# Kernel tuning notes

Measured on AMD Instinct MI355X. Metric: run time of the kernel, lower is better.

Reference implementation:

```python
import jax, jax.numpy as jnp
import numpy as np

N, IN_DIM, D, H, E_DIM, G, NPG = 512, 16, 256, 8, 6, 32, 16
C = D           # per-head channels in GATv2Conv/TransformerConv (out_channels=d_model)
HD = D // H     # MultiheadAttention head dim


def _ln(x, g, b, eps=1e-5):
    m = jnp.mean(x, -1, keepdims=True)
    v = jnp.mean((x - m) ** 2, -1, keepdims=True)
    return (x - m) * jax.lax.rsqrt(v + eps) * g + b


def _seg_softmax(logits, seg, n):
    # numerically stable softmax over edges grouped by destination node
    m = jax.ops.segment_max(logits, seg, num_segments=n)
    m = jnp.where(jnp.isfinite(m), m, 0.0)
    e = jnp.exp(logits - m[seg])
    s = jax.ops.segment_sum(e, seg, num_segments=n)
    return e / jnp.maximum(s[seg], 1e-16)


def _forward(x, edge_attr, emb_w, emb_b, emb_g, emb_bb, pe, gat_lw, gat_lb, gat_rw, gat_rb, gat_ew, gat_att, gat_bias, tq_w, tq_b, tk_w, tk_b, tv_w, tv_b, te_w, tskip_w, tskip_b, tbeta_w, ln_g, ln_b, mha_in_w, mha_in_b, mha_out_w, mha_out_b, pool_w, pool_b, c1_w, c1_b, c1_g, c1_bb, rb_w, rb_b, rb_g, rb_bb, c2_w, c2_b, edge_index, batch):
    src, dst = edge_index[0], edge_index[1]
    E = edge_attr.shape[0]
    # input embedding (Linear + LayerNorm) + learned positional encoding (eval: no dropout)
    h = _ln(x @ emb_w.T + emb_b, emb_g, emb_bb) + pe[:N]
    residual = h
    # --- GATv2Conv(d_model, d_model, heads=H, edge_dim=6, concat=False, add_self_loops=False) ---
    xl = (h @ gat_lw.T + gat_lb).reshape(N, H, C)          # source transform
    xr = (h @ gat_rw.T + gat_rb).reshape(N, H, C)          # target transform
    ee = (edge_attr @ gat_ew.T).reshape(E, H, C)
    z = jax.nn.leaky_relu(xl[src] + xr[dst] + ee, 0.2)
    a = _seg_softmax(jnp.einsum('ehc,hc->eh', z, gat_att), dst, N)
    x_gat = jax.ops.segment_sum(xl[src] * a[..., None], dst, num_segments=N).mean(1) + gat_bias
    x_gat = _ln(x_gat, ln_g, ln_b)
    # --- TransformerConv(d_model, d_model, heads=H, edge_dim=6, concat=False, beta=True) ---
    te = (edge_attr @ te_w.T).reshape(E, H, C)
    q = (x_gat @ tq_w.T + tq_b).reshape(N, H, C)[dst]
    k = (x_gat @ tk_w.T + tk_b).reshape(N, H, C)[src] + te
    v = (x_gat @ tv_w.T + tv_b).reshape(N, H, C)[src] + te
    a2 = _seg_softmax((q * k).sum(-1) / np.sqrt(C).astype(np.float32), dst, N)
    out = jax.ops.segment_sum(v * a2[..., None], dst, num_segments=N).mean(1)
    r = x_gat @ tskip_w.T + tskip_b
    beta = jax.nn.sigmoid(jnp.concatenate([out, r, out - r], -1) @ tbeta_w.T)
    x_tr = _ln(beta * r + (1.0 - beta) * out, ln_g, ln_b)
    # --- dynamic attention mask: after the repeat/permute/reshape gymnastics this equals
    #     ds[:N] repeated H*N times, reshaped to [H, N, N] ---
    im = edge_attr[:, 5]
    ds = jnp.exp(-0.5 * ((im - 125.09) / 15.0) ** 2)
    ds = 1.0 - (ds - ds.min()) / (ds.max() - ds.min())
    mask = jnp.repeat(ds[:N], H * N).reshape(H, N, N)
    # --- cross MultiheadAttention (query=x_tr, key=x_gat, value=h, attn_mask added) ---
    wq, wk, wv = jnp.split(mha_in_w, 3, axis=0)
    bq, bk, bv = jnp.split(mha_in_b, 3, axis=0)
    qh = ((x_tr @ wq.T + bq) / np.sqrt(HD).astype(np.float32)).reshape(N, H, HD).transpose(1, 0, 2)
    kh = (x_gat @ wk.T + bk).reshape(N, H, HD).transpose(1, 0, 2)
    vh = (h @ wv.T + bv).reshape(N, H, HD).transpose(1, 0, 2)
    attn = jax.nn.softmax(qh @ kh.transpose(0, 2, 1) + mask, axis=-1)   # [H,N,N]
    o = (attn @ vh).transpose(1, 0, 2).reshape(N, D) @ mha_out_w.T + mha_out_b
    # torch broadcast of [N,1,D] attn output + [N,D] residual -> [N,N,D]
    x3 = o[:, None, :] + residual[None, :, :]
    # attention pooling: softmax over a size-1 dim yields all-ones scores (kept faithfully)
    x2 = x3.reshape(N * N, D)
    brep = jnp.tile(batch, N)
    score = jax.nn.softmax(x2 @ pool_w.T + pool_b, axis=1)
    pooled = jax.ops.segment_sum(score * x2, brep, num_segments=G)
    # classifier: Linear->LN->GELU->ResidualBlockv2->Linear (dropout off in eval)
    c = jax.nn.gelu(_ln(pooled @ c1_w.T + c1_b, c1_g, c1_bb), approximate=False)
    c = c + jax.nn.gelu(_ln(c @ rb_w.T + rb_b, rb_g, rb_bb), approximate=False)
    return c @ c2_w.T + c2_b   # [G, 1]


def setup_inputs():
    key = jax.random.key(0)
    ks = iter(jax.random.split(key, 64))
    f = lambda *sh: 0.02 * jax.random.normal(next(ks), sh, jnp.float32)
    # G fully-connected directed cliques of NPG nodes (no self loops) -> every node has in-edges
    i = np.arange(NPG)
    s, t = np.meshgrid(i, i, indexing='ij')
    msk = s != t
    s, t = s[msk], t[msk]
    off = (np.arange(G) * NPG)[:, None]
    edge_index = jnp.asarray(np.stack([(s[None] + off).reshape(-1), (t[None] + off).reshape(-1)]), jnp.int32)
    E = edge_index.shape[1]
    batch = jnp.asarray(np.repeat(np.arange(G), NPG), jnp.int32)
    x = jax.random.normal(next(ks), (N, IN_DIM), jnp.float32)
    edge_attr = jax.random.normal(next(ks), (E, E_DIM), jnp.float32)
    edge_attr = edge_attr.at[:, 5].set(edge_attr[:, 5] * 30.0 + 125.0)  # invariant-mass-like column
    HC = H * C
    return dict(
        x=x, edge_attr=edge_attr,
        emb_w=f(D, IN_DIM), emb_b=f(D), emb_g=jnp.ones(D), emb_bb=jnp.zeros(D),
        pe=f(1000, D),
        gat_lw=f(HC, D), gat_lb=f(HC), gat_rw=f(HC, D), gat_rb=f(HC),
        gat_ew=f(HC, E_DIM), gat_att=f(H, C), gat_bias=f(C),
        tq_w=f(HC, D), tq_b=f(HC), tk_w=f(HC, D), tk_b=f(HC),
        tv_w=f(HC, D), tv_b=f(HC), te_w=f(HC, E_DIM),
        tskip_w=f(D, D), tskip_b=f(D), tbeta_w=f(1, 3 * D),
        ln_g=jnp.ones(D), ln_b=jnp.zeros(D),
        mha_in_w=f(3 * D, D), mha_in_b=f(3 * D), mha_out_w=f(D, D), mha_out_b=f(D),
        pool_w=f(1, D), pool_b=f(1),
        c1_w=f(128, D), c1_b=f(128), c1_g=jnp.ones(128), c1_bb=jnp.zeros(128),
        rb_w=f(128, 128), rb_b=f(128), rb_g=jnp.ones(128), rb_bb=jnp.zeros(128),
        c2_w=f(1, 128), c2_b=f(1),
        edge_index=edge_index, batch=batch)


def reference(x, edge_attr, emb_w, emb_b, emb_g, emb_bb, pe, gat_lw, gat_lb, gat_rw, gat_rb, gat_ew, gat_att, gat_bias, tq_w, tq_b, tk_w, tk_b, tv_w, tv_b, te_w, tskip_w, tskip_b, tbeta_w, ln_g, ln_b, mha_in_w, mha_in_b, mha_out_w, mha_out_b, pool_w, pool_b, c1_w, c1_b, c1_g, c1_bb, rb_w, rb_b, rb_g, rb_bb, c2_w, c2_b, edge_index, batch):
    return _forward(x, edge_attr, emb_w, emb_b, emb_g, emb_bb, pe, gat_lw, gat_lb, gat_rw, gat_rb, gat_ew, gat_att, gat_bias, tq_w, tq_b, tk_w, tk_b, tv_w, tv_b, te_w, tskip_w, tskip_b, tbeta_w, ln_g, ln_b, mha_in_w, mha_in_b, mha_out_w, mha_out_b, pool_w, pool_b, c1_w, c1_b, c1_g, c1_bb, rb_w, rb_b, rb_g, rb_bb, c2_w, c2_b, edge_index, batch)
```

## Files before the change

### kernel.cpp

```cpp
#include <hip/hip_runtime.h>
#include <hip/hip_bf16.h>
#include <math.h>

#define NN 512
#define DM 256
#define NH 8
#define NG 32
#define NPG 16
#define INDIM 16
#define BIGW (2048 * 256)

typedef __hip_bfloat16 bf16;
typedef __attribute__((ext_vector_type(8))) short short8;
typedef __attribute__((ext_vector_type(4))) float f32x4;

__device__ __forceinline__ float b2f(bf16 v) { return __bfloat162float(v); }
__device__ __forceinline__ bf16 f2b(float v) { return __float2bfloat16(v); }
__device__ __forceinline__ short f2bs(float v) { bf16 t = __float2bfloat16(v); return *(short*)&t; }
__device__ __forceinline__ float fin(float v) {
    return (v == v && v > -1e30f && v < 1e30f) ? v : 0.f;
}
__device__ __forceinline__ int is_bf16(const void* ones_arr) {
    return ((const unsigned short*)ones_arr)[0] == 0x3F80u;
}

__device__ __forceinline__ void unpack8(uint4 u, float* w) {
    unsigned uu[4] = {u.x, u.y, u.z, u.w};
    #pragma unroll
    for (int j = 0; j < 4; j++) {
        __hip_bfloat162 b2 = *reinterpret_cast<const __hip_bfloat162*>(&uu[j]);
        float2 f = __bfloat1622float2(b2);
        w[2 * j] = f.x; w[2 * j + 1] = f.y;
    }
}
__device__ __forceinline__ float4 bload4(const bf16* p) {
    uint2 u = *(const uint2*)p;
    __hip_bfloat162 a = *reinterpret_cast<const __hip_bfloat162*>(&u.x);
    __hip_bfloat162 b = *reinterpret_cast<const __hip_bfloat162*>(&u.y);
    float2 f0 = __bfloat1622float2(a), f1 = __bfloat1622float2(b);
    return make_float4(f0.x, f0.y, f1.x, f1.y);
}

__device__ __forceinline__ float dot256(const float* xrow, const bf16* wrow) {
    const uint4* w4 = (const uint4*)wrow;
    uint4 q = w4[0];
    float acc = 0.f;
    for (int k8 = 0; k8 < 32; k8++) {
        uint4 qn = w4[(k8 + 1) & 31];
        float w[8]; unpack8(q, w);
        const float4* sp = (const float4*)&xrow[k8 * 8];
        float4 a0 = sp[0], a1 = sp[1];
        acc += a0.x*w[0] + a0.y*w[1] + a0.z*w[2] + a0.w*w[3]
             + a1.x*w[4] + a1.y*w[5] + a1.z*w[6] + a1.w*w[7];
        q = qn;
    }
    return acc;
}

template<int BS>
__device__ __forceinline__ float ln_norm(float v, float g, float b, float* red) {
    int t = threadIdx.x;
    red[t] = v; __syncthreads();
    for (int s = BS / 2; s > 0; s >>= 1) { if (t < s) red[t] += red[t + s]; __syncthreads(); }
    float mean = red[0] * (1.0f / (float)BS); __syncthreads();
    float d = v - mean;
    red[t] = d * d; __syncthreads();
    for (int s = BS / 2; s > 0; s >>= 1) { if (t < s) red[t] += red[t + s]; __syncthreads(); }
    float var = red[0] * (1.0f / (float)BS); __syncthreads();
    return d * rsqrtf(var + 1e-5f) * g + b;
}

struct CvtTab { const void* p[35]; int cum[36]; };
__global__ void k_convert(CvtTab tab, const void* ones, bf16* wbuf) {
    int i = blockIdx.x * 256 + threadIdx.x;
    if (i >= tab.cum[35]) return;
    int bf = is_bf16(ones);
    int a = 0;
    while (i >= tab.cum[a + 1]) a++;
    int off = i - tab.cum[a];
    float v = bf ? b2f(((const bf16*)tab.p[a])[off]) : ((const float*)tab.p[a])[off];
    wbuf[i] = f2b(v);
}

struct Cvt5 { const void* p[5]; };
__global__ void k_convert_big(Cvt5 tab, const void* ones, bf16* wbig) {
    int i = blockIdx.x * 256 + threadIdx.x;
    int a = blockIdx.y;
    int bf = is_bf16(ones);
    float v = bf ? b2f(((const bf16*)tab.p[a])[i]) : ((const float*)tab.p[a])[i];
    wbig[(size_t)a * BIGW + i] = f2b(v);
}

__global__ void k_embed(const bf16* xw, const bf16* emw, const bf16* emb, const bf16* emg,
                        const bf16* embb, const bf16* pe, float* h,
                        float* pre1, float* pre2) {
    int n = blockIdx.x, t = threadIdx.x;
    size_t gi = (size_t)n * DM + t;
    pre1[gi] = 0.f;
    pre2[gi] = 0.f;
    __shared__ float xin[INDIM];
    __shared__ float red[DM];
    if (t < INDIM) xin[t] = b2f(xw[n * INDIM + t]);
    __syncthreads();
    float acc = b2f(emb[t]);
    #pragma unroll
    for (int k = 0; k < INDIM; k++) acc += xin[k] * b2f(emw[t * INDIM + k]);
    float y = ln_norm<DM>(acc, b2f(emg[t]), b2f(embb[t]), red);
    h[gi] = fin(y + b2f(pe[gi]));
}

__device__ __forceinline__ void row_softmax16(float* M, int tid) {
    if (tid < NPG) {
        float* row = M + tid * NPG;
        float m = -1e30f;
        #pragma unroll
        for (int s = 0; s < NPG; s++) m = fmaxf(m, row[s]);
        if (m < -1e29f) {
            #pragma unroll
            for (int s = 0; s < NPG; s++) row[s] = 0.f;
        } else {
            float sum = 0.f;
            #pragma unroll
            for (int s = 0; s < NPG; s++) sum += expf(row[s] - m);
            float inv = 1.f / fmaxf(sum, 1e-16f);
            #pragma unroll
            for (int s = 0; s < NPG; s++) row[s] = expf(row[s] - m) * inv;
        }
    }
}

__global__ __launch_bounds__(256, 1)
void k_gat_fused(const float* h, const bf16* lw, const bf16* rw,
                 const bf16* lb, const bf16* rbv, const bf16* eww, const bf16* attw,
                 const bf16* ea, const int* src, const int* dst, int epg, float* pre) {
    extern __shared__ char smraw[];
    int g = blockIdx.x, hh = blockIdx.y, tid = threadIdx.x;
    bf16* hb     = (bf16*)smraw;
    float* ew_s  = (float*)(hb + NPG * DM);
    float* att_s = ew_s + 6 * DM;
    float* ea_s  = att_s + DM;
    float* Mx    = ea_s + 6 * epg;
    int* sl_s    = (int*)(Mx + NPG * NPG);
    int* dl_s    = sl_s + epg;
    bf16* xl_s   = (bf16*)(dl_s + epg);
    bf16* xr_s   = xl_s + NPG * DM;

    int ebase = g * epg;
    for (int i = tid; i < NPG * DM; i += 256) hb[i] = f2b(h[(size_t)g * NPG * DM + i]);
    for (int i = tid; i < 6 * DM; i += 256) {
        int f = i >> 8, cc = i & 255;
        ew_s[f * DM + cc] = b2f(eww[(size_t)(hh * DM + cc) * 6 + f]);
    }
    att_s[tid] = b2f(attw[hh * DM + tid]);
    for (int i = tid; i < 6 * epg; i += 256) {
        int f = i / epg, e = i - f * epg;
        ea_s[f * epg + e] = b2f(ea[(size_t)(ebase + e) * 6 + f]);
    }
    if (tid < NPG * NPG) Mx[tid] = -1e30f;
    if (tid < epg) {
        int e = ebase + tid;
        sl_s[tid] = (src[e] - g * NPG) & (NPG - 1);
        dl_s[tid] = (dst[e] - g * NPG) & (NPG - 1);
    }
    __syncthreads();

    int lane = tid & 63, wave = tid >> 6;
    int n16 = lane & 15, quad = lane >> 4;
    f32x4 accA[4], accB[4];
    #pragma unroll
    for (int ct = 0; ct < 4; ct++) { accA[ct] = (f32x4)0.f; accB[ct] = (f32x4)0.f; }
    for (int ks = 0; ks < 8; ks++) {
        short8 a8 = *(const short8*)&hb[n16 * DM + ks * 32 + quad * 8];
        #pragma unroll
        for (int ct = 0; ct < 4; ct++) {
            int col = (ct * 4 + wave) * 16 + n16;
            size_t wo = (size_t)(hh * DM + col) * DM + ks * 32 + quad * 8;
            short8 bL = *(const short8*)(lw + wo);
            short8 bR = *(const short8*)(rw + wo);
            accA[ct] = __builtin_amdgcn_mfma_f32_16x16x32_bf16(a8, bL, accA[ct], 0, 0, 0);
            accB[ct] = __builtin_amdgcn_mfma_f32_16x16x32_bf16(a8, bR, accB[ct], 0, 0, 0);
        }
    }
    #pragma unroll
    for (int ct = 0; ct < 4; ct++) {
        int col = (ct * 4 + wave) * 16 + n16;
        float blv = b2f(lb[hh * DM + col]), brv = b2f(rbv[hh * DM + col]);
        #pragma unroll
        for (int reg = 0; reg < 4; reg++) {
            int row = quad * 4 + reg;
            xl_s[row * DM + col] = f2b(accA[ct][reg] + blv);
            xr_s[row * DM + col] = f2b(accB[ct][reg] + brv);
        }
    }
    __syncthreads();

    int c4 = lane * 4;
    for (int ei = wave; ei < epg; ei += 4) {
        int sl = sl_s[ei], dl = dl_s[ei];
        float ee0 = 0.f, ee1 = 0.f, ee2 = 0.f, ee3 = 0.f;
        #pragma unroll
        for (int f = 0; f < 6; f++) {
            float eb = ea_s[f * epg + ei];
            float4 wf = *(const float4*)&ew_s[f * DM + c4];
            ee0 += eb * wf.x; ee1 += eb * wf.y; ee2 += eb * wf.z; ee3 += eb * wf.w;
        }
        float4 av = *(const float4*)&att_s[c4];
        float4 xlv = bload4(&xl_s[sl * DM + c4]);
        float4 xrv = bload4(&xr_s[dl * DM + c4]);
        float z0 = xlv.x + xrv.x + ee0;
        float z1 = xlv.y + xrv.y + ee1;
        float z2 = xlv.z + xrv.z + ee2;
        float z3 = xlv.w + xrv.w + ee3;
        z0 = (z0 >= 0.f) ? z0 : 0.2f * z0;
        z1 = (z1 >= 0.f) ? z1 : 0.2f * z1;
        z2 = (z2 >= 0.f) ? z2 : 0.2f * z2;
        z3 = (z3 >= 0.f) ? z3 : 0.2f * z3;
        float acc = z0 * av.x + z1 * av.y + z2 * av.z + z3 * av.w;
        #pragma unroll
        for (int off = 32; off > 0; off >>= 1) acc += __shfl_down(acc, off);
        if (lane == 0) Mx[dl * NPG + sl] = fin(acc);
    }
    __syncthreads();
    row_softmax16(Mx, tid);
    __syncthreads();

    int c = tid;
    float xlv[NPG];
    #pragma unroll
    for (int s = 0; s < NPG; s++) xlv[s] = b2f(xl_s[s * DM + c]);
    #pragma unroll
    for (int d = 0; d < NPG; d++) {
        const float* Ar = Mx + d * NPG;
        float acc = 0.f;
        #pragma unroll
        for (int s = 0; s < NPG; s++) acc += Ar[s] * xlv[s];
        atomicAdd(&pre[(size_t)(g * NPG + d) * DM + c], fin(acc));
    }
}

__global__ void k_gat_post_skip(const float* pre, const bf16* gat_bias, const bf16* lng,
                                const bf16* lnb, const bf16* skw, const bf16* skb,
                                float* x_gat, float* rbuf) {
    int n = blockIdx.x, t = threadIdx.x;
    __shared__ float red[DM];
    __shared__ float xrow[DM];
    float v = pre[(size_t)n * DM + t] * 0.125f + b2f(gat_bias[t]);
    float y = fin(ln_norm<DM>(v, b2f(lng[t]), b2f(lnb[t]), red));
    x_gat[(size_t)n * DM + t] = y;
    xrow[t] = y;
    __syncthreads();
    rbuf[(size_t)n * DM + t] = fin(dot256(xrow, skw + (size_t)t * DM) + b2f(skb[t]));
}

__global__ __launch_bounds__(256, 1)
void k_tr_fused(const float* xg, const bf16* qw, const bf16* kw, const bf16* vw,
                const bf16* qb, const bf16* kb, const bf16* vb, const bf16* tew,
                const bf16* ea, const int* src, const int* dst, int epg, float* pre) {
    extern __shared__ char smraw[];
    int g = blockIdx.x, hh = blockIdx.y, tid = threadIdx.x;
    bf16* hb    = (bf16*)smraw;
    float* tw_s = (float*)(hb + NPG * DM);
    float* ea_s = tw_s + 6 * DM;
    float* Lqk  = ea_s + 6 * epg;
    float* Mx   = Lqk + NPG * NPG;
    float* P    = Mx + NPG * NPG;
    float* W6   = P + NPG * 6;
    int* emap   = (int*)(W6 + NPG * 6);
    int* sl_s   = emap + NPG * NPG;
    int* dl_s   = sl_s + epg;
    bf16* q_s   = (bf16*)(dl_s + epg);
    bf16* k_s   = q_s + NPG * DM;
    bf16* v_s   = k_s + NPG * DM;

    int ebase = g * epg;
    for (int i = tid; i < NPG * DM; i += 256) hb[i] = f2b(xg[(size_t)g * NPG * DM + i]);
    for (int i = tid; i < 6 * DM; i += 256) {
        int f = i >> 8, cc = i & 255;
        tw_s[f * DM + cc] = b2f(tew[(size_t)(hh * DM + cc) * 6 + f]);
    }
    for (int i = tid; i < 6 * epg; i += 256) {
        int f = i / epg, e = i - f * epg;
        ea_s[f * epg + e] = b2f(ea[(size_t)(ebase + e) * 6 + f]);
    }
    if (tid < NPG * NPG) { Mx[tid] = -1e30f; emap[tid] = -1; }
    if (tid < epg) {
        int e = ebase + tid;
        sl_s[tid] = (src[e] - g * NPG) & (NPG - 1);
        dl_s[tid] = (dst[e] - g * NPG) & (NPG - 1);
    }
    __syncthreads();

    int lane = tid & 63, wave = tid >> 6;
    int n16 = lane & 15, quad = lane >> 4;
    f32x4 aQ[4], aK[4], aV[4];
    #pragma unroll
    for (int ct = 0; ct < 4; ct++) { aQ[ct] = (f32x4)0.f; aK[ct] = (f32x4)0.f; aV[ct] = (f32x4)0.f; }
    for (int ks = 0; ks < 8; ks++) {
        short8 a8 = *(const short8*)&hb[n16 * DM + ks * 32 + quad * 8];
        #pragma unroll
        for (int ct = 0; ct < 4; ct++) {
            int col = (ct * 4 + wave) * 16 + n16;
            size_t wo = (size_t)(hh * DM + col) * DM + ks * 32 + quad * 8;
            short8 bQ = *(const short8*)(qw + wo);
            short8 bK = *(const short8*)(kw + wo);
            short8 bV = *(const short8*)(vw + wo);
            aQ[ct] = __builtin_amdgcn_mfma_f32_16x16x32_bf16(a8, bQ, aQ[ct], 0, 0, 0);
            aK[ct] = __builtin_amdgcn_mfma_f32_16x16x32_bf16(a8, bK, aK[ct], 0, 0, 0);
            aV[ct] = __builtin_amdgcn_mfma_f32_16x16x32_bf16(a8, bV, aV[ct], 0, 0, 0);
        }
    }
    #pragma unroll
    for (int ct = 0; ct < 4; ct++) {
        int col = (ct * 4 + wave) * 16 + n16;
        float bq = b2f(qb[hh * DM + col]), bk = b2f(kb[hh * DM + col]), bv = b2f(vb[hh * DM + col]);
        #pragma unroll
        for (int reg = 0; reg < 4; reg++) {
            int row = quad * 4 + reg;
            q_s[row * DM + col] = f2b(aQ[ct][reg] + bq);
            k_s[row * DM + col] = f2b(aK[ct][reg] + bk);
            v_s[row * DM + col] = f2b(aV[ct][reg] + bv);
        }
    }
    __syncthreads();

    if (wave == 0) {
        f32x4 acc = (f32x4)0.f;
        for (int ks = 0; ks < 8; ks++) {
            short8 a8 = *(const short8*)&q_s[n16 * DM + ks * 32 + quad * 8];
            short8 b8 = *(const short8*)&k_s[n16 * DM + ks * 32 + quad * 8];
            acc = __builtin_amdgcn_mfma_f32_16x16x32_bf16(a8, b8, acc, 0, 0, 0);
        }
        #pragma unroll
        for (int reg = 0; reg < 4; reg++)
            Lqk[(quad * 4 + reg) * NPG + n16] = acc[reg];
    } else if (wave <= 2) {
        int idx = tid - 64;
        if (idx < NPG * 6) {
            int d = idx / 6, f = idx - d * 6;
            const bf16* qr = q_s + d * DM;
            const float* twr = tw_s + f * DM;
            float acc = 0.f;
            for (int cc = 0; cc < DM; cc += 4) {
                float4 qv = bload4(qr + cc);
                float4 t4 = *(const float4*)(twr + cc);
                acc += qv.x * t4.x + qv.y * t4.y + qv.z * t4.z + qv.w * t4.w;
            }
            P[idx] = acc;
        }
    }
    __syncthreads();

    if (tid < epg) {
        int sl = sl_s[tid], dl = dl_s[tid];
        float acc = Lqk[dl * NPG + sl];
        #pragma unroll
        for (int f = 0; f < 6; f++) acc += ea_s[f * epg + tid] * P[dl * 6 + f];
        Mx[dl * NPG + sl] = fin(acc * 0.0625f);
        emap[dl * NPG + sl] = tid;
    }
    __syncthreads();
    row_softmax16(Mx, tid);
    __syncthreads();
    if (tid < NPG * 6) {
        int d = tid / 6, f = tid - d * 6;
        float acc = 0.f;
        #pragma unroll
        for (int s = 0; s < NPG; s++) {
            int e = emap[d * NPG + s];
            if (e >= 0) acc += Mx[d * NPG + s] * ea_s[f * epg + e];
        }
        W6[tid] = acc;
    }
    __syncthreads();

    int c = tid;
    float vv[NPG];
    #pragma unroll
    for (int s = 0; s < NPG; s++) vv[s] = b2f(v_s[s * DM + c]);
    float twc[6];
    #pragma unroll
    for (int f = 0; f < 6; f++) twc[f] = tw_s[f * DM + c];
    #pragma unroll
    for (int d = 0; d < NPG; d++) {
        const float* Ar = Mx + d * NPG;
        const float* Wr = W6 + d * 6;
        float acc = 0.f;
        #pragma unroll
        for (int s = 0; s < NPG; s++) acc += Ar[s] * vv[s];
        #pragma unroll
        for (int f = 0; f < 6; f++) acc += Wr[f] * twc[f];
        atomicAdd(&pre[(size_t)(g * NPG + d) * DM + c], fin(acc));
    }
}

__global__ void k_tr_post_qkv(const float* pre, const float* rbuf, const float* x_gat,
                              const float* h, const bf16* tbeta, const bf16* lng,
                              const bf16* lnb, const bf16* mw, const bf16* mb, float* qkv) {
    int n = blockIdx.x, t = threadIdx.x;
    __shared__ float red[DM];
    __shared__ float xtr_s[DM];
    __shared__ float xg_s[DM];
    __shared__ float h_s[DM];
    __shared__ float beta_sh;
    float outc = pre[(size_t)n * DM + t] * 0.125f;
    float rc = rbuf[(size_t)n * DM + t];
    xg_s[t] = x_gat[(size_t)n * DM + t];
    h_s[t] = h[(size_t)n * DM + t];
    float w1 = b2f(tbeta[t]), w2 = b2f(tbeta[DM + t]), w3 = b2f(tbeta[2 * DM + t]);
    red[t] = outc * (w1 + w3) + rc * (w2 - w3);
    __syncthreads();
    for (int s2 = 128; s2 > 0; s2 >>= 1) { if (t < s2) red[t] += red[t + s2]; __syncthreads(); }
    if (t == 0) beta_sh = 1.0f / (1.0f + expf(-red[0]));
    __syncthreads();
    float beta = beta_sh;
    float mix = beta * rc + (1.0f - beta) * outc;
    float y = fin(ln_norm<DM>(mix, b2f(lng[t]), b2f(lnb[t]), red));
    xtr_s[t] = y;
    __syncthreads();
    float q = (dot256(xtr_s, mw + (size_t)t * DM) + b2f(mb[t])) * 0.17677669529663689f;
    float k = dot256(xg_s, mw + (size_t)(DM + t) * DM) + b2f(mb[DM + t]);
    float v = dot256(h_s, mw + (size_t)(2 * DM + t) * DM) + b2f(mb[2 * DM + t]);
    qkv[(size_t)n * DM + t] = fin(q);
    qkv[((size_t)NN + n) * DM + t] = fin(k);
    qkv[((size_t)2 * NN + n) * DM + t] = fin(v);
}

#define KPAD 40
#define SPAD 516
__global__ __launch_bounds__(256, 1)
void k_attn(const float* qh, const float* kh, const float* vh, float* ao) {
    extern __shared__ char sm[];
    bf16* qb   = (bf16*)sm;
    bf16* KV   = qb + 16 * 32;
    float* Sc  = (float*)(KV + 256 * KPAD);
    float* Op  = Sc + 16 * SPAD;
    float* red = Op + 4 * 16 * 32;
    int qt = blockIdx.x, hd = blockIdx.y, tid = threadIdx.x;
    int lane = tid & 63, wave = tid >> 6, n16 = lane & 15, quad = lane >> 4;

    for (int i = tid; i < 16 * 32; i += 256)
        qb[i] = f2b(qh[(size_t)(qt * 16 + (i >> 5)) * DM + hd * 32 + (i & 31)]);

    for (int half = 0; half < 2; half++) {
        __syncthreads();
        for (int i = tid; i < 256 * 32; i += 256) {
            int j = i >> 5, d = i & 31;
            KV[j * KPAD + d] = f2b(kh[(size_t)(half * 256 + j) * DM + hd * 32 + d]);
        }
        __syncthreads();
        short8 a8 = *(const short8*)&qb[n16 * 32 + quad * 8];
        #pragma unroll
        for (int it = 0; it < 4; it++) {
            int ktl = wave * 4 + it;
            short8 b8 = *(const short8*)&KV[(ktl * 16 + n16) * KPAD + quad * 8];
            f32x4 acc = (f32x4)0.f;
            acc = __builtin_amdgcn_mfma_f32_16x16x32_bf16(a8, b8, acc, 0, 0, 0);
            #pragma unroll
            for (int reg = 0; reg < 4; reg++)
                Sc[(quad * 4 + reg) * SPAD + half * 256 + ktl * 16 + n16] = acc[reg];
        }
    }
    __syncthreads();

    int r = tid >> 4, li = tid & 15;
    float m = -1e30f;
    for (int s = 0; s < 32; s++) m = fmaxf(m, Sc[r * SPAD + li + 16 * s]);
    red[r * 16 + li] = m; __syncthreads();
    for (int st = 8; st > 0; st >>= 1) {
        if (li < st) red[r * 16 + li] = fmaxf(red[r * 16 + li], red[r * 16 + li + st]);
        __syncthreads();
    }
    m = red[r * 16];
    __syncthreads();
    float sum = 0.f;
    for (int s = 0; s < 32; s++) sum += expf(Sc[r * SPAD + li + 16 * s] - m);
    red[r * 16 + li] = sum; __syncthreads();
    for (int st = 8; st > 0; st >>= 1) {
        if (li < st) red[r * 16 + li] += red[r * 16 + li + st];
        __syncthreads();
    }
    float inv = 1.0f / fmaxf(red[r * 16], 1e-16f);
    for (int s = 0; s < 32; s++) {
        int idx = r * SPAD + li + 16 * s;
        Sc[idx] = expf(Sc[idx] - m) * inv;
    }

    f32x4 o0 = (f32x4)0.f, o1 = (f32x4)0.f;
    for (int half = 0; half < 2; half++) {
        __syncthreads();
        for (int i = tid; i < 256 * 32; i += 256) {
            int j = i >> 5, d = i & 31;
            KV[j * KPAD + d] = f2b(vh[(size_t)(half * 256 + j) * DM + hd * 32 + d]);
        }
        __syncthreads();
        #pragma unroll
        for (int it = 0; it < 2; it++) {
            int ksl = wave * 2 + it;
            int ks = half * 8 + ksl;
            const float* sp = &Sc[n16 * SPAD + ks * 32 + quad * 8];
            float4 s0 = *(const float4*)sp, s1 = *((const float4*)sp + 1);
            short8 a8;
            a8[0] = f2bs(s0.x); a8[1] = f2bs(s0.y); a8[2] = f2bs(s0.z); a8[3] = f2bs(s0.w);
            a8[4] = f2bs(s1.x); a8[5] = f2bs(s1.y); a8[6] = f2bs(s1.z); a8[7] = f2bs(s1.w);
            short8 bv0, bv1;
            #pragma unroll
            for (int j = 0; j < 8; j++) {
                bf16 t0 = KV[(ksl * 32 + quad * 8 + j) * KPAD + n16];
                bf16 t1 = KV[(ksl * 32 + quad * 8 + j) * KPAD + 16 + n16];
                bv0[j] = *(short*)&t0;
                bv1[j] = *(short*)&t1;
            }
            o0 = __builtin_amdgcn_mfma_f32_16x16x32_bf16(a8, bv0, o0, 0, 0, 0);
            o1 = __builtin_amdgcn_mfma_f32_16x16x32_bf16(a8, bv1, o1, 0, 0, 0);
        }
    }
    #pragma unroll
    for (int reg = 0; reg < 4; reg++) {
        Op[wave * 512 + (quad * 4 + reg) * 32 + n16] = o0[reg];
        Op[wave * 512 + (quad * 4 + reg) * 32 + 16 + n16] = o1[reg];
    }
    __syncthreads();
    for (int e = tid; e < 512; e += 256) {
        float v = Op[e] + Op[512 + e] + Op[1024 + e] + Op[1536 + e];
        ao[(size_t)(qt * 16 + (e >> 5)) * DM + hd * 32 + (e & 31)] = fin(v);
    }
}

__global__ void k_outproj(const float* ao, const bf16* W, const bf16* B, float* obuf) {
    int n = blockIdx.x, t = threadIdx.x;
    __shared__ float xrow[DM];
    xrow[t] = ao[(size_t)n * DM + t];
    __syncthreads();
    obuf[(size_t)n * DM + t] = fin(dot256(xrow, W + (size_t)t * DM) + b2f(B[t]));
}

__global__ void k_pool_sums(const float* o, const float* h, float* gsum_o, float* gsum_h) {
    int g = blockIdx.x, which = blockIdx.y, t = threadIdx.x;
    const float* src = which ? h : o;
    float acc = 0.f;
    #pragma unroll
    for (int j = 0; j < NPG; j++) acc += src[(size_t)(g * NPG + j) * DM + t];
    (which ? gsum_h : gsum_o)[g * DM + t] = fin(acc);
}

__global__ void k_mlp(const float* gsum_o, const float* gsum_h,
                      const bf16* c1_w, const bf16* c1_b, const bf16* c1_g,
                      const bf16* c1_bb, const bf16* rb_w, const bf16* rb_b,
                      const bf16* rb_g, const bf16* rb_bb, const bf16* c2_w,
                      const bf16* c2_b, const void* ones, void* out) {
    int g = blockIdx.x, t = threadIdx.x;
    __shared__ float pl[DM];
    __shared__ float u[128];
    __shared__ float red[128];
    float os0 = 0.f, os1 = 0.f;
    #pragma unroll
    for (int b = 0; b < NG; b++) {
        os0 += gsum_o[b * DM + t];
        os1 += gsum_o[b * DM + t + 128];
    }
    pl[t]       = fin((float)NPG * os0 + (float)NN * gsum_h[g * DM + t]);
    pl[t + 128] = fin((float)NPG * os1 + (float)NN * gsum_h[g * DM + t + 128]);
    __syncthreads();
    float acc = dot256(pl, c1_w + (size_t)t * DM) + b2f(c1_b[t]);
    float y = ln_norm<128>(acc, b2f(c1_g[t]), b2f(c1_bb[t]), red);
    float gl = 0.5f * y * (1.0f + erff(y * 0.70710678118654752f));
    u[t] = gl; __syncthreads();
    float acc2 = b2f(rb_b[t]);
    for (int k = 0; k < 128; k++) acc2 += u[k] * b2f(rb_w[(size_t)t * 128 + k]);
    float y2 = ln_norm<128>(acc2, b2f(rb_g[t]), b2f(rb_bb[t]), red);
    float cfin = gl + 0.5f * y2 * (1.0f + erff(y2 * 0.70710678118654752f));
    red[t] = cfin * b2f(c2_w[t]);
    __syncthreads();
    for (int s2 = 64; s2 > 0; s2 >>= 1) { if (t < s2) red[t] += red[t + s2]; __syncthreads(); }
    if (t == 0) {
        float res = fin(red[0] + b2f(c2_b[0]));
        if (is_bf16(ones)) ((bf16*)out)[g] = f2b(res);
        else               ((float*)out)[g] = res;
    }
}

extern "C" void kernel_launch(void* const* d_in, const int* in_sizes, int n_in,
                              void* d_out, int out_size, void* d_ws, size_t ws_size,
                              hipStream_t stream) {
    const int E = in_sizes[1] / 6;
    const int epg = E / NG;
    const int* eidx = (const int*)d_in[42];
    const int* srcp = eidx;
    const int* dstp = eidx + E;
    const void* ones = d_in[4];

    static const int idxs[35] = {0,1,2,3,4,5,6,8,10,11,12,13,15,17,19,20,21,22,23,24,
                                 25,26,27,28,29,32,33,34,35,36,37,38,39,40,41};
    CvtTab tab;
    int wOff[44];
    int cum = 0;
    for (int a = 0; a < 35; a++) {
        tab.p[a] = d_in[idxs[a]];
        tab.cum[a] = cum;
        wOff[idxs[a]] = cum;
        cum += in_sizes[idxs[a]];
    }
    tab.cum[35] = cum;
    const int totalW = cum;
    Cvt5 tab5;
    tab5.p[0] = d_in[7];  tab5.p[1] = d_in[9];
    tab5.p[2] = d_in[14]; tab5.p[3] = d_in[16]; tab5.p[4] = d_in[18];

    bf16* wbuf = (bf16*)d_ws;
    size_t wbytes = ((size_t)totalW * 2 + 255) & ~(size_t)255;
    float* fb = (float*)((char*)d_ws + wbytes);
    const size_t SL = (size_t)NN * DM;
    float* h      = fb;
    float* x_gat  = fb + SL;
    float* rbuf   = fb + 2 * SL;
    float* pre1   = fb + 3 * SL;
    float* pre2   = fb + 4 * SL;
    float* qkv    = fb + 5 * SL;
    float* gsum_o = fb + 8 * SL;
    float* gsum_h = gsum_o + NG * DM;
    bf16* wbig = (bf16*)qkv;
    float* ao = pre1;
    float* obuf = pre2;

    #define WB(i) (wbuf + wOff[i])

    k_convert<<<(totalW + 255) / 256, 256, 0, stream>>>(tab, ones, wbuf);
    k_convert_big<<<dim3(BIGW / 256, 5), 256, 0, stream>>>(tab5, ones, wbig);

    k_embed<<<NN, DM, 0, stream>>>(WB(0), WB(2), WB(3), WB(4), WB(5), WB(6), h, pre1, pre2);

    int gat_lds = NPG*DM*2 + (6*DM + DM + 6*epg + NPG*NPG) * 4 + (2*epg) * 4
                + 2*NPG*DM*2 + 16;
    k_gat_fused<<<dim3(NG, NH), 256, gat_lds, stream>>>(
        h, wbig, wbig + BIGW, WB(8), WB(10), WB(11), WB(12), WB(1), srcp, dstp, epg, pre1);
    k_gat_post_skip<<<NN, DM, 0, stream>>>(pre1, WB(13), WB(24), WB(25), WB(21), WB(22),
                                           x_gat, rbuf);

    int tr_lds = NPG*DM*2 + (6*DM + 6*epg + 2*NPG*NPG + 2*NPG*6) * 4
               + (NPG*NPG + 2*epg) * 4 + 3*NPG*DM*2 + 16;
    k_tr_fused<<<dim3(NG, NH), 256, tr_lds, stream>>>(
        x_gat, wbig + 2 * (size_t)BIGW, wbig + 3 * (size_t)BIGW, wbig + 4 * (size_t)BIGW,
        WB(15), WB(17), WB(19), WB(20), WB(1), srcp, dstp, epg, pre2);
    k_tr_post_qkv<<<NN, DM, 0, stream>>>(pre2, rbuf, x_gat, h, WB(23), WB(24), WB(25),
                                         WB(26), WB(27), qkv);

    int attn_lds = 16*32*2 + 256*KPAD*2 + 16*SPAD*4 + 4*16*32*4 + 16*16*4;
    k_attn<<<dim3(NN / 16, NH), 256, attn_lds, stream>>>(qkv, qkv + SL, qkv + 2 * SL, ao);
    k_outproj<<<NN, DM, 0, stream>>>(ao, WB(28), WB(29), obuf);

    k_pool_sums<<<dim3(NG, 2), DM, 0, stream>>>(obuf, h, gsum_o, gsum_h);
    k_mlp<<<NG, 128, 0, stream>>>(gsum_o, gsum_h, WB(32), WB(33), WB(34), WB(35),
                                  WB(36), WB(37), WB(38), WB(39), WB(40), WB(41),
                                  ones, d_out);
    #undef WB
}
```

Baseline: 321.7 us.

## Double GAT/Transformer conv block threads and fold pooling sums into producers

The fused GAT and TransformerConv kernels now launch 512 threads per block instead of 256. The MFMA column tiles, edge loop and aggregation loop are split across 8 waves, and the edge and attention weights are kept in LDS as bf16 to shrink shared memory. The separate pooling-sum kernel is removed: per-graph sums of h and of the output projection are accumulated with atomicAdd in the embed and outproj kernels, and the accumulators are zeroed inside the convert kernel. This cuts one launch and raises per-block parallelism, at the cost of atomic contention and non-deterministic summation order.

```diff
diff --git a/kernel.cpp b/kernel.cpp
--- a/kernel.cpp
+++ b/kernel.cpp
@@ -71,15 +71,18 @@
 }
 
 struct CvtTab { const void* p[35]; int cum[36]; };
-__global__ void k_convert(CvtTab tab, const void* ones, bf16* wbuf) {
+__global__ void k_convert(CvtTab tab, const void* ones, bf16* wbuf, float* gz, int nz) {
     int i = blockIdx.x * 256 + threadIdx.x;
-    if (i >= tab.cum[35]) return;
-    int bf = is_bf16(ones);
-    int a = 0;
-    while (i >= tab.cum[a + 1]) a++;
-    int off = i - tab.cum[a];
-    float v = bf ? b2f(((const bf16*)tab.p[a])[off]) : ((const float*)tab.p[a])[off];
-    wbuf[i] = f2b(v);
+    if (i < tab.cum[35]) {
+        int bf = is_bf16(ones);
+        int a = 0;
+        while (i >= tab.cum[a + 1]) a++;
+        int off = i - tab.cum[a];
+        float v = bf ? b2f(((const bf16*)tab.p[a])[off]) : ((const float*)tab.p[a])[off];
+        wbuf[i] = f2b(v);
+    } else if (i < tab.cum[35] + nz) {
+        gz[i - tab.cum[35]] = 0.f;
+    }
 }
 
 struct Cvt5 { const void* p[5]; };
@@ -93,7 +96,7 @@
 
 __global__ void k_embed(const bf16* xw, const bf16* emw, const bf16* emb, const bf16* emg,
                         const bf16* embb, const bf16* pe, float* h,
-                        float* pre1, float* pre2) {
+                        float* pre1, float* pre2, float* gsum_h) {
     int n = blockIdx.x, t = threadIdx.x;
     size_t gi = (size_t)n * DM + t;
     pre1[gi] = 0.f;
@@ -106,7 +109,9 @@
     #pragma unroll
     for (int k = 0; k < INDIM; k++) acc += xin[k] * b2f(emw[t * INDIM + k]);
     float y = ln_norm<DM>(acc, b2f(emg[t]), b2f(embb[t]), red);
-    h[gi] = fin(y + b2f(pe[gi]));
+    float hv = fin(y + b2f(pe[gi]));
+    h[gi] = hv;
+    atomicAdd(&gsum_h[(n >> 4) * DM + t], hv);
 }
 
 __device__ __forceinline__ void row_softmax16(float* M, int tid) {
@@ -129,16 +134,16 @@
     }
 }
 
-__global__ __launch_bounds__(256, 1)
+__global__ __launch_bounds__(512, 1)
 void k_gat_fused(const float* h, const bf16* lw, const bf16* rw,
                  const bf16* lb, const bf16* rbv, const bf16* eww, const bf16* attw,
                  const bf16* ea, const int* src, const int* dst, int epg, float* pre) {
     extern __shared__ char smraw[];
     int g = blockIdx.x, hh = blockIdx.y, tid = threadIdx.x;
     bf16* hb     = (bf16*)smraw;
-    float* ew_s  = (float*)(hb + NPG * DM);
-    float* att_s = ew_s + 6 * DM;
-    float* ea_s  = att_s + DM;
+    bf16* ew_s   = hb + NPG * DM;
+    bf16* att_s  = ew_s + 6 * DM;
+    float* ea_s  = (float*)(att_s + DM);
     float* Mx    = ea_s + 6 * epg;
     int* sl_s    = (int*)(Mx + NPG * NPG);
     int* dl_s    = sl_s + epg;
@@ -146,13 +151,13 @@
     bf16* xr_s   = xl_s + NPG * DM;
 
     int ebase = g * epg;
-    for (int i = tid; i < NPG * DM; i += 256) hb[i] = f2b(h[(size_t)g * NPG * DM + i]);
-    for (int i = tid; i < 6 * DM; i += 256) {
+    for (int i = tid; i < NPG * DM; i += 512) hb[i] = f2b(h[(size_t)g * NPG * DM + i]);
+    for (int i = tid; i < 6 * DM; i += 512) {
         int f = i >> 8, cc = i & 255;
-        ew_s[f * DM + cc] = b2f(eww[(size_t)(hh * DM + cc) * 6 + f]);
-    }
-    att_s[tid] = b2f(attw[hh * DM + tid]);
-    for (int i = tid; i < 6 * epg; i += 256) {
+        ew_s[f * DM + cc] = eww[(size_t)(hh * DM + cc) * 6 + f];
+    }
+    if (tid < DM) att_s[tid] = attw[hh * DM + tid];
+    for (int i = tid; i < 6 * epg; i += 512) {
         int f = i / epg, e = i - f * epg;
         ea_s[f * epg + e] = b2f(ea[(size_t)(ebase + e) * 6 + f]);
     }
@@ -166,14 +171,14 @@
 
     int lane = tid & 63, wave = tid >> 6;
     int n16 = lane & 15, quad = lane >> 4;
-    f32x4 accA[4], accB[4];
-    #pragma unroll
-    for (int ct = 0; ct < 4; ct++) { accA[ct] = (f32x4)0.f; accB[ct] = (f32x4)0.f; }
+    f32x4 accA[2], accB[2];
+    #pragma unroll
+    for (int ct = 0; ct < 2; ct++) { accA[ct] = (f32x4)0.f; accB[ct] = (f32x4)0.f; }
     for (int ks = 0; ks < 8; ks++) {
         short8 a8 = *(const short8*)&hb[n16 * DM + ks * 32 + quad * 8];
         #pragma unroll
-        for (int ct = 0; ct < 4; ct++) {
-            int col = (ct * 4 + wave) * 16 + n16;
+        for (int ct = 0; ct < 2; ct++) {
+            int col = (ct * 8 + wave) * 16 + n16;
             size_t wo = (size_t)(hh * DM + col) * DM + ks * 32 + quad * 8;
             short8 bL = *(const short8*)(lw + wo);
             short8 bR = *(const short8*)(rw + wo);
@@ -182,8 +187,8 @@
         }
     }
     #pragma unroll
-    for (int ct = 0; ct < 4; ct++) {
-        int col = (ct * 4 + wave) * 16 + n16;
+    for (int ct = 0; ct < 2; ct++) {
+        int col = (ct * 8 + wave) * 16 + n16;
         float blv = b2f(lb[hh * DM + col]), brv = b2f(rbv[hh * DM + col]);
         #pragma unroll
         for (int reg = 0; reg < 4; reg++) {
@@ -195,16 +200,16 @@
     __syncthreads();
 
     int c4 = lane * 4;
-    for (int ei = wave; ei < epg; ei += 4) {
+    for (int ei = wave; ei < epg; ei += 8) {
         int sl = sl_s[ei], dl = dl_s[ei];
         float ee0 = 0.f, ee1 = 0.f, ee2 = 0.f, ee3 = 0.f;
         #pragma unroll
         for (int f = 0; f < 6; f++) {
             float eb = ea_s[f * epg + ei];
-            float4 wf = *(const float4*)&ew_s[f * DM + c4];
+            float4 wf = bload4(&ew_s[f * DM + c4]);
             ee0 += eb * wf.x; ee1 += eb * wf.y; ee2 += eb * wf.z; ee3 += eb * wf.w;
         }
-        float4 av = *(const float4*)&att_s[c4];
+        float4 av = bload4(&att_s[c4]);
         float4 xlv = bload4(&xl_s[sl * DM + c4]);
         float4 xrv = bload4(&xr_s[dl * DM + c4]);
         float z0 = xlv.x + xrv.x + ee0;
@@ -224,12 +229,13 @@
     row_softmax16(Mx, tid);
     __syncthreads();
 
-    int c = tid;
+    int c = tid & 255, halfd = tid >> 8;
     float xlv[NPG];
     #pragma unroll
     for (int s = 0; s < NPG; s++) xlv[s] = b2f(xl_s[s * DM + c]);
     #pragma unroll
-    for (int d = 0; d < NPG; d++) {
+    for (int dd = 0; dd < 8; dd++) {
+        int d = halfd * 8 + dd;
         const float* Ar = Mx + d * NPG;
         float acc = 0.f;
         #pragma unroll
@@ -252,15 +258,15 @@
     rbuf[(size_t)n * DM + t] = fin(dot256(xrow, skw + (size_t)t * DM) + b2f(skb[t]));
 }
 
-__global__ __launch_bounds__(256, 1)
+__global__ __launch_bounds__(512, 1)
 void k_tr_fused(const float* xg, const bf16* qw, const bf16* kw, const bf16* vw,
                 const bf16* qb, const bf16* kb, const bf16* vb, const bf16* tew,
                 const bf16* ea, const int* src, const int* dst, int epg, float* pre) {
     extern __shared__ char smraw[];
     int g = blockIdx.x, hh = blockIdx.y, tid = threadIdx.x;
     bf16* hb    = (bf16*)smraw;
-    float* tw_s = (float*)(hb + NPG * DM);
-    float* ea_s = tw_s + 6 * DM;
+    bf16* tw_s  = hb + NPG * DM;
+    float* ea_s = (float*)(tw_s + 6 * DM);
     float* Lqk  = ea_s + 6 * epg;
     float* Mx   = Lqk + NPG * NPG;
     float* P    = Mx + NPG * NPG;
@@ -273,12 +279,12 @@
     bf16* v_s   = k_s + NPG * DM;
 
     int ebase = g * epg;
-    for (int i = tid; i < NPG * DM; i += 256) hb[i] = f2b(xg[(size_t)g * NPG * DM + i]);
-    for (int i = tid; i < 6 * DM; i += 256) {
+    for (int i = tid; i < NPG * DM; i += 512) hb[i] = f2b(xg[(size_t)g * NPG * DM + i]);
+    for (int i = tid; i < 6 * DM; i += 512) {
         int f = i >> 8, cc = i & 255;
-        tw_s[f * DM + cc] = b2f(tew[(size_t)(hh * DM + cc) * 6 + f]);
-    }
-    for (int i = tid; i < 6 * epg; i += 256) {
+        tw_s[f * DM + cc] = tew[(size_t)(hh * DM + cc) * 6 + f];
+    }
+    for (int i = tid; i < 6 * epg; i += 512) {
         int f = i / epg, e = i - f * epg;
         ea_s[f * epg + e] = b2f(ea[(size_t)(ebase + e) * 6 + f]);
     }
@@ -292,14 +298,14 @@
 
     int lane = tid & 63, wave = tid >> 6;
     int n16 = lane & 15, quad = lane >> 4;
-    f32x4 aQ[4], aK[4], aV[4];
-    #pragma unroll
-    for (int ct = 0; ct < 4; ct++) { aQ[ct] = (f32x4)0.f; aK[ct] = (f32x4)0.f; aV[ct] = (f32x4)0.f; }
+    f32x4 aQ[2], aK[2], aV[2];
+    #pragma unroll
+    for (int ct = 0; ct < 2; ct++) { aQ[ct] = (f32x4)0.f; aK[ct] = (f32x4)0.f; aV[ct] = (f32x4)0.f; }
     for (int ks = 0; ks < 8; ks++) {
         short8 a8 = *(const short8*)&hb[n16 * DM + ks * 32 + quad * 8];
         #pragma unroll
-        for (int ct = 0; ct < 4; ct++) {
-            int col = (ct * 4 + wave) * 16 + n16;
+        for (int ct = 0; ct < 2; ct++) {
+            int col = (ct * 8 + wave) * 16 + n16;
             size_t wo = (size_t)(hh * DM + col) * DM + ks * 32 + quad * 8;
             short8 bQ = *(const short8*)(qw + wo);
             short8 bK = *(const short8*)(kw + wo);
@@ -310,8 +316,8 @@
         }
     }
     #pragma unroll
-    for (int ct = 0; ct < 4; ct++) {
-        int col = (ct * 4 + wave) * 16 + n16;
+    for (int ct = 0; ct < 2; ct++) {
+        int col = (ct * 8 + wave) * 16 + n16;
         float bq = b2f(qb[hh * DM + col]), bk = b2f(kb[hh * DM + col]), bv = b2f(vb[hh * DM + col]);
         #pragma unroll
         for (int reg = 0; reg < 4; reg++) {
@@ -338,11 +344,11 @@
         if (idx < NPG * 6) {
             int d = idx / 6, f = idx - d * 6;
             const bf16* qr = q_s + d * DM;
-            const float* twr = tw_s + f * DM;
+            const bf16* twr = tw_s + f * DM;
             float acc = 0.f;
             for (int cc = 0; cc < DM; cc += 4) {
                 float4 qv = bload4(qr + cc);
-                float4 t4 = *(const float4*)(twr + cc);
+                float4 t4 = bload4(twr + cc);
                 acc += qv.x * t4.x + qv.y * t4.y + qv.z * t4.z + qv.w * t4.w;
             }
             P[idx] = acc;
@@ -373,15 +379,16 @@
     }
     __syncthreads();
 
-    int c = tid;
+    int c = tid & 255, halfd = tid >> 8;
     float vv[NPG];
     #pragma unroll
     for (int s = 0; s < NPG; s++) vv[s] = b2f(v_s[s * DM + c]);
     float twc[6];
     #pragma unroll
-    for (int f = 0; f < 6; f++) twc[f] = tw_s[f * DM + c];
-    #pragma unroll
-    for (int d = 0; d < NPG; d++) {
+    for (int f = 0; f < 6; f++) twc[f] = b2f(tw_s[f * DM + c]);
+    #pragma unroll
+    for (int dd = 0; dd < 8; dd++) {
+        int d = halfd * 8 + dd;
         const float* Ar = Mx + d * NPG;
         const float* Wr = W6 + d * 6;
         float acc = 0.f;
@@ -526,21 +533,15 @@
     }
 }
 
-__global__ void k_outproj(const float* ao, const bf16* W, const bf16* B, float* obuf) {
+__global__ void k_outproj(const float* ao, const bf16* W, const bf16* B,
+                          float* obuf, float* gsum_o) {
     int n = blockIdx.x, t = threadIdx.x;
     __shared__ float xrow[DM];
     xrow[t] = ao[(size_t)n * DM + t];
     __syncthreads();
-    obuf[(size_t)n * DM + t] = fin(dot256(xrow, W + (size_t)t * DM) + b2f(B[t]));
-}
-
-__global__ void k_pool_sums(const float* o, const float* h, float* gsum_o, float* gsum_h) {
-    int g = blockIdx.x, which = blockIdx.y, t = threadIdx.x;
-    const float* src = which ? h : o;
-    float acc = 0.f;
-    #pragma unroll
-    for (int j = 0; j < NPG; j++) acc += src[(size_t)(g * NPG + j) * DM + t];
-    (which ? gsum_h : gsum_o)[g * DM + t] = fin(acc);
+    float v = fin(dot256(xrow, W + (size_t)t * DM) + b2f(B[t]));
+    obuf[(size_t)n * DM + t] = v;
+    atomicAdd(&gsum_o[(n >> 4) * DM + t], v);
 }
 
 __global__ void k_mlp(const float* gsum_o, const float* gsum_h,
@@ -621,24 +622,26 @@
     bf16* wbig = (bf16*)qkv;
     float* ao = pre1;
     float* obuf = pre2;
+    const int NZ = 2 * NG * DM;
 
     #define WB(i) (wbuf + wOff[i])
 
-    k_convert<<<(totalW + 255) / 256, 256, 0, stream>>>(tab, ones, wbuf);
+    k_convert<<<(totalW + NZ + 255) / 256, 256, 0, stream>>>(tab, ones, wbuf, gsum_o, NZ);
     k_convert_big<<<dim3(BIGW / 256, 5), 256, 0, stream>>>(tab5, ones, wbig);
 
-    k_embed<<<NN, DM, 0, stream>>>(WB(0), WB(2), WB(3), WB(4), WB(5), WB(6), h, pre1, pre2);
-
-    int gat_lds = NPG*DM*2 + (6*DM + DM + 6*epg + NPG*NPG) * 4 + (2*epg) * 4
+    k_embed<<<NN, DM, 0, stream>>>(WB(0), WB(2), WB(3), WB(4), WB(5), WB(6), h,
+                                   pre1, pre2, gsum_h);
+
+    int gat_lds = NPG*DM*2 + 6*DM*2 + DM*2 + (6*epg + NPG*NPG + 2*epg) * 4
                 + 2*NPG*DM*2 + 16;
-    k_gat_fused<<<dim3(NG, NH), 256, gat_lds, stream>>>(
+    k_gat_fused<<<dim3(NG, NH), 512, gat_lds, stream>>>(
         h, wbig, wbig + BIGW, WB(8), WB(10), WB(11), WB(12), WB(1), srcp, dstp, epg, pre1);
     k_gat_post_skip<<<NN, DM, 0, stream>>>(pre1, WB(13), WB(24), WB(25), WB(21), WB(22),
                                            x_gat, rbuf);
 
-    int tr_lds = NPG*DM*2 + (6*DM + 6*epg + 2*NPG*NPG + 2*NPG*6) * 4
+    int tr_lds = NPG*DM*2 + 6*DM*2 + (6*epg + 2*NPG*NPG + 2*NPG*6) * 4
                + (NPG*NPG + 2*epg) * 4 + 3*NPG*DM*2 + 16;
-    k_tr_fused<<<dim3(NG, NH), 256, tr_lds, stream>>>(
+    k_tr_fused<<<dim3(NG, NH), 512, tr_lds, stream>>>(
         x_gat, wbig + 2 * (size_t)BIGW, wbig + 3 * (size_t)BIGW, wbig + 4 * (size_t)BIGW,
         WB(15), WB(17), WB(19), WB(20), WB(1), srcp, dstp, epg, pre2);
     k_tr_post_qkv<<<NN, DM, 0, stream>>>(pre2, rbuf, x_gat, h, WB(23), WB(24), WB(25),
@@ -646,9 +649,8 @@
 
     int attn_lds = 16*32*2 + 256*KPAD*2 + 16*SPAD*4 + 4*16*32*4 + 16*16*4;
     k_attn<<<dim3(NN / 16, NH), 256, attn_lds, stream>>>(qkv, qkv + SL, qkv + 2 * SL, ao);
-    k_outproj<<<NN, DM, 0, stream>>>(ao, WB(28), WB(29), obuf);
-
-    k_pool_sums<<<dim3(NG, 2), DM, 0, stream>>>(obuf, h, gsum_o, gsum_h);
+    k_outproj<<<NN, DM, 0, stream>>>(ao, WB(28), WB(29), obuf, gsum_o);
+
     k_mlp<<<NG, 128, 0, stream>>>(gsum_o, gsum_h, WB(32), WB(33), WB(34), WB(35),
                                   WB(36), WB(37), WB(38), WB(39), WB(40), WB(41),
                                   ones, d_out);
```

Result: faster. 304.3 us (-5.4%).
